# Performance work log

Measured on AMD Instinct MI355X. Metric: run time of the kernel, lower is better.

Reference implementation:

```python
import jax, jax.numpy as jnp
import numpy as np

LAMBDA = 25.0
MU = 25.0
NU = 1.0
ALPHA = 0.25
EPS = 1e-4
NUM_MATCHES = (20, 4)


def _cdist(x, y):
    # x: (B, L1, C), y: (B, L2, C) -> (B, L1, L2) euclidean distances
    x2 = jnp.sum(x * x, axis=-1)[..., :, None]
    y2 = jnp.sum(y * y, axis=-1)[..., None, :]
    d2 = x2 + y2 - 2.0 * jnp.einsum('blc,bmc->blm', x, y)
    return jnp.sqrt(jnp.maximum(d2, 0.0))


def _nearest_neighbors(input_maps, candidate_maps, distances, num_matches):
    # For each input location, its nearest candidate; then keep the
    # num_matches input locations with smallest NN distance, in original order.
    nn_dist = jnp.min(distances, axis=-1)    # (B, L1)
    nn_idx = jnp.argmin(distances, axis=-1)  # (B, L1)
    _, sel = jax.lax.top_k(-nn_dist, num_matches)  # (B, M) smallest distances
    sel = jnp.sort(sel, axis=1)  # restore original ordering of positions
    filtered_input = jnp.take_along_axis(input_maps, sel[..., None], axis=1)
    nn_sel = jnp.take_along_axis(nn_idx, sel, axis=1)
    filtered_candidate = jnp.take_along_axis(candidate_maps, nn_sel[..., None], axis=1)
    return filtered_input, filtered_candidate


def _mse(a, b):
    return jnp.mean((a - b) ** 2)


def _vicreg_loss(z_a, z_b):
    inv_loss = _mse(z_a, z_b)

    def var_loss(z):
        std = jnp.sqrt(jnp.var(z, axis=0, ddof=1) + EPS)
        return jnp.mean(jax.nn.relu(1.0 - std))

    def cov_loss(z):
        n, d = z.shape
        zc = z - jnp.mean(z, axis=0)
        cov = (zc.T @ zc) / (n - 1)
        off = cov - jnp.diag(jnp.diag(cov))
        return jnp.sum(off ** 2) / d

    v = 0.5 * (var_loss(z_a) + var_loss(z_b))
    c = cov_loss(z_a) + cov_loss(z_b)
    return LAMBDA * inv_loss + MU * v + NU * c


def _local_loss(z_global, z_local, grid_global, grid_local):
    B = z_global.shape[0]
    zg = z_global.reshape(B, -1, z_global.shape[-1])   # (B, Lg, C)
    zl = z_local.reshape(B, -1, z_local.shape[-1])     # (B, Ll, C)

    inv_loss = 0.0
    # feature-space NN
    gf, gn = _nearest_neighbors(zg, zl, _cdist(zg, zl), NUM_MATCHES[0])
    lf, ln = _nearest_neighbors(zl, zg, _cdist(zl, zg), NUM_MATCHES[1])
    inv_loss = inv_loss + (_mse(gf, gn) / 2 + _mse(lf, ln) / 2)

    # grid-space NN (distances from grids, gather from feature maps)
    gg = grid_global.reshape(B, -1, 2)
    gl = grid_local.reshape(B, -1, 2)
    gf, gn = _nearest_neighbors(zg, zl, _cdist(gg, gl), NUM_MATCHES[0])
    lf, ln = _nearest_neighbors(zl, zg, _cdist(gl, gg), NUM_MATCHES[1])
    inv_loss = inv_loss + (_mse(gf, gn) / 2 + _mse(lf, ln) / 2)

    return LAMBDA * inv_loss


def setup_inputs() -> dict:
    key = jax.random.key(0)
    ks = jax.random.split(key, 6)
    B, D, C = 32, 8192, 512
    return {
        'z_global': jax.random.normal(ks[0], (B, D), jnp.float32),
        'z_local': jax.random.normal(ks[1], (B, D), jnp.float32),
        'z_global_local_features': jax.random.normal(ks[2], (B, 24, 24, C), jnp.float32),
        'z_local_local_features': jax.random.normal(ks[3], (B, 16, 16, C), jnp.float32),
        'grid_global': jax.random.uniform(ks[4], (B, 24, 24, 2), jnp.float32),
        'grid_local': jax.random.uniform(ks[5], (B, 16, 16, 2), jnp.float32),
    }


def reference(z_global, z_local, z_global_local_features, z_local_local_features, grid_global, grid_local):
    global_loss = _vicreg_loss(z_global, z_local)
    local_loss = _local_loss(z_global_local_features, z_local_local_features, grid_global, grid_local)
    return ALPHA * global_loss + (1.0 - ALPHA) * local_loss
```

## Files before the change

### kernel.cpp

```cpp
#include <hip/hip_runtime.h>
#include <hip/hip_bf16.h>

#define BATCH 32
#define DZ    8192
#define LG    576
#define LL    256
#define CH    512

#define OFF_S      0
#define OFF_BSUM   8192
#define OFF_SELSUM 9472
#define OFF_NG     10496
#define OFF_NL     84224
#define OFF_ROWNN  116992
#define OFF_COLNN  264448
#define OFF_ABF    329984
#define OFF_BBF    19204352
#define WS_NEED    27592960

typedef __attribute__((ext_vector_type(8))) short bf16x8;
typedef __attribute__((ext_vector_type(4))) float f32x4;

__device__ __forceinline__ unsigned short f2bf(float x) {
  union { __hip_bfloat16 h; unsigned short u; } cv;
  cv.h = __float2bfloat16(x);
  return cv.u;
}

__global__ __launch_bounds__(256) void k_stats_gram(
    const float* __restrict__ za, const float* __restrict__ zb,
    double* __restrict__ bsum, float* __restrict__ S) {
  __shared__ float sred[4][5];
  int tid = threadIdx.x, lane = tid & 63, wv = tid >> 6;
  int blk = blockIdx.x;
  if (blk < 32) {
    int i = blk * 256 + tid;
    float sa = 0.f, qa = 0.f, sb = 0.f, qb = 0.f, si = 0.f;
    #pragma unroll 8
    for (int b = 0; b < BATCH; ++b) {
      float va = za[(size_t)b * DZ + i];
      float vb = zb[(size_t)b * DZ + i];
      sa += va; qa += va * va;
      sb += vb; qb += vb * vb;
      float d = va - vb; si += d * d;
    }
    float ssa = qa - sa * sa * (1.f / 32.f);
    float ssb = qb - sb * sb * (1.f / 32.f);
    float v0 = si;
    float v1 = fmaxf(0.f, 1.f - sqrtf(ssa * (1.f / 31.f) + 1e-4f));
    float v2 = fmaxf(0.f, 1.f - sqrtf(ssb * (1.f / 31.f) + 1e-4f));
    float v3 = ssa * ssa, v4 = ssb * ssb;
    for (int off = 32; off; off >>= 1) {
      v0 += __shfl_down(v0, off); v1 += __shfl_down(v1, off);
      v2 += __shfl_down(v2, off); v3 += __shfl_down(v3, off);
      v4 += __shfl_down(v4, off);
    }
    if (lane == 0) {
      sred[wv][0] = v0; sred[wv][1] = v1; sred[wv][2] = v2;
      sred[wv][3] = v3; sred[wv][4] = v4;
    }
    __syncthreads();
    if (tid < 5)
      bsum[blk * 5 + tid] =
          (double)(sred[0][tid] + sred[1][tid] + sred[2][tid] + sred[3][tid]);
  } else {
    int e = blk - 32;
    int zi = e >= 528; if (zi) e -= 528;
    const float* z = zi ? zb : za;
    float* Sz = S + zi * 1024;
    int p = 0, rem = e;
    while (rem >= 32 - p) { rem -= 32 - p; ++p; }
    int q = p + rem;
    const float4* zp = (const float4*)(z + (size_t)p * DZ);
    const float4* zq = (const float4*)(z + (size_t)q * DZ);
    float s = 0.f;
    #pragma unroll
    for (int ii = 0; ii < 8; ++ii) {
      int i = tid + ii * 256;
      float4 a = zp[i], b = zq[i];
      s += a.x * b.x + a.y * b.y + a.z * b.z + a.w * b.w;
    }
    for (int off = 32; off; off >>= 1) s += __shfl_down(s, off);
    if (lane == 0) sred[wv][0] = s;
    __syncthreads();
    if (tid == 0) {
      float r = sred[0][0] + sred[1][0] + sred[2][0] + sred[3][0];
      Sz[p * 32 + q] = r;
      if (p != q) Sz[q * 32 + p] = r;
    }
  }
}

__global__ __launch_bounds__(256) void k_prep(
    const float* __restrict__ zgf, const float* __restrict__ zlf,
    unsigned short* __restrict__ Abf, unsigned short* __restrict__ Bbf,
    float* __restrict__ ng, float* __restrict__ nl,
    unsigned long long* __restrict__ nnInit) {
  int row = blockIdx.x * 4 + (threadIdx.x >> 6);
  int lane = threadIdx.x & 63;
  if (lane == 0) nnInit[row] = ~0ull;
  const float* src; unsigned short* dst; float* nrm;
  if (row < BATCH * LG) {
    src = zgf + (size_t)row * CH; dst = Abf + (size_t)row * CH; nrm = ng + row;
  } else {
    int rr = row - BATCH * LG;
    src = zlf + (size_t)rr * CH; dst = Bbf + (size_t)rr * CH; nrm = nl + rr;
  }
  const float4* s4 = (const float4*)src;
  float4 v0 = s4[lane * 2], v1 = s4[lane * 2 + 1];
  float ss = v0.x * v0.x + v0.y * v0.y + v0.z * v0.z + v0.w * v0.w +
             v1.x * v1.x + v1.y * v1.y + v1.z * v1.z + v1.w * v1.w;
  union { unsigned short h[8]; uint4 u; } pk;
  pk.h[0] = f2bf(v0.x); pk.h[1] = f2bf(v0.y); pk.h[2] = f2bf(v0.z); pk.h[3] = f2bf(v0.w);
  pk.h[4] = f2bf(v1.x); pk.h[5] = f2bf(v1.y); pk.h[6] = f2bf(v1.z); pk.h[7] = f2bf(v1.w);
  *(uint4*)(dst + lane * 8) = pk.u;
  for (int off = 32; off; off >>= 1) ss += __shfl_down(ss, off);
  if (lane == 0) *nrm = ss;
}

__global__ __launch_bounds__(256) void k_feat_mfma(
    const unsigned short* __restrict__ Abf, const unsigned short* __restrict__ Bbf,
    const float* __restrict__ ng, const float* __restrict__ nl,
    unsigned long long* __restrict__ rowNN, unsigned long long* __restrict__ colNN) {
  const int b = blockIdx.z;
  const int row0 = blockIdx.x * 64;
  const int col0 = blockIdx.y * 64;
  const int tid = threadIdx.x;
  const int wave = tid >> 6, lane = tid & 63;
  const int m16 = lane & 15, quad = lane >> 4;
  const int wm = wave >> 1, wn = wave & 1;

  __shared__ unsigned short As[64][72];
  __shared__ unsigned short Bs[64][72];

  const unsigned short* Ag = Abf + ((size_t)(b * LG + row0)) * CH;
  const unsigned short* Bg = Bbf + ((size_t)(b * LL + col0)) * CH;

  const int sr = tid >> 2;
  const int sq = tid & 3;

  f32x4 acc[2][2] = {};

  for (int k0 = 0; k0 < CH; k0 += 64) {
    uint4 a0 = *(const uint4*)(Ag + (size_t)sr * CH + k0 + sq * 16);
    uint4 a1 = *(const uint4*)(Ag + (size_t)sr * CH + k0 + sq * 16 + 8);
    uint4 b0 = *(const uint4*)(Bg + (size_t)sr * CH + k0 + sq * 16);
    uint4 b1 = *(const uint4*)(Bg + (size_t)sr * CH + k0 + sq * 16 + 8);
    __syncthreads();
    *(uint4*)&As[sr][sq * 16] = a0; *(uint4*)&As[sr][sq * 16 + 8] = a1;
    *(uint4*)&Bs[sr][sq * 16] = b0; *(uint4*)&Bs[sr][sq * 16 + 8] = b1;
    __syncthreads();
    #pragma unroll
    for (int kk = 0; kk < 64; kk += 32) {
      bf16x8 af0 = *(const bf16x8*)&As[wm * 32 + m16][kk + quad * 8];
      bf16x8 af1 = *(const bf16x8*)&As[wm * 32 + 16 + m16][kk + quad * 8];
      bf16x8 bf0 = *(const bf16x8*)&Bs[wn * 32 + m16][kk + quad * 8];
      bf16x8 bf1 = *(const bf16x8*)&Bs[wn * 32 + 16 + m16][kk + quad * 8];
      acc[0][0] = __builtin_amdgcn_mfma_f32_16x16x32_bf16(af0, bf0, acc[0][0], 0, 0, 0);
      acc[0][1] = __builtin_amdgcn_mfma_f32_16x16x32_bf16(af0, bf1, acc[0][1], 0, 0, 0);
      acc[1][0] = __builtin_amdgcn_mfma_f32_16x16x32_bf16(af1, bf0, acc[1][0], 0, 0, 0);
      acc[1][1] = __builtin_amdgcn_mfma_f32_16x16x32_bf16(af1, bf1, acc[1][1], 0, 0, 0);
    }
  }

  float na[2][4], nb[2];
  #pragma unroll
  for (int i = 0; i < 2; ++i)
    #pragma unroll
    for (int r = 0; r < 4; ++r)
      na[i][r] = ng[b * LG + row0 + wm * 32 + i * 16 + quad * 4 + r];
  #pragma unroll
  for (int j = 0; j < 2; ++j)
    nb[j] = nl[b * LL + col0 + wn * 32 + j * 16 + m16];

  #pragma unroll
  for (int i = 0; i < 2; ++i) {
    #pragma unroll
    for (int r = 0; r < 4; ++r) {
      float d0 = fmaxf(na[i][r] + nb[0] - 2.f * acc[i][0][r], 0.f);
      float d1 = fmaxf(na[i][r] + nb[1] - 2.f * acc[i][1][r], 0.f);
      unsigned c0 = (unsigned)(col0 + wn * 32 + m16);
      unsigned long long p0 = (((unsigned long long)__float_as_uint(d0)) << 32) | c0;
      unsigned long long p1 = (((unsigned long long)__float_as_uint(d1)) << 32) | (c0 + 16);
      unsigned long long p = p0 < p1 ? p0 : p1;
      #pragma unroll
      for (int s = 1; s < 16; s <<= 1) {
        unsigned long long q = __shfl_xor(p, s);
        p = q < p ? q : p;
      }
      if (m16 == 0)
        atomicMin(&rowNN[(size_t)b * LG + row0 + wm * 32 + i * 16 + quad * 4 + r], p);
    }
  }
  #pragma unroll
  for (int j = 0; j < 2; ++j) {
    unsigned long long p = ~0ull;
    #pragma unroll
    for (int i = 0; i < 2; ++i) {
      #pragma unroll
      for (int r = 0; r < 4; ++r) {
        float d = fmaxf(na[i][r] + nb[j] - 2.f * acc[i][j][r], 0.f);
        unsigned rg = (unsigned)(row0 + wm * 32 + i * 16 + quad * 4 + r);
        unsigned long long pr = (((unsigned long long)__float_as_uint(d)) << 32) | rg;
        p = pr < p ? pr : p;
      }
    }
    unsigned long long q = __shfl_xor(p, 16); p = q < p ? q : p;
    q = __shfl_xor(p, 32); p = q < p ? q : p;
    if (quad == 0)
      atomicMin(&colNN[(size_t)b * LL + col0 + wn * 32 + j * 16 + m16], p);
  }
}

__global__ __launch_bounds__(64) void k_norms(
    const float* __restrict__ zgf, const float* __restrict__ zlf,
    float* __restrict__ ng, float* __restrict__ nl,
    unsigned long long* __restrict__ nnInit) {
  int r = blockIdx.x;
  if (threadIdx.x == 0) nnInit[r] = ~0ull;
  const float* src; float* dst;
  if (r < BATCH * LG) { src = zgf + (size_t)r * CH; dst = ng + r; }
  else { int rr = r - BATCH * LG; src = zlf + (size_t)rr * CH; dst = nl + rr; }
  float s = 0.f;
  for (int j = threadIdx.x; j < CH; j += 64) { float v = src[j]; s += v * v; }
  for (int off = 32; off > 0; off >>= 1) s += __shfl_down(s, off);
  if (threadIdx.x == 0) *dst = s;
}

__global__ __launch_bounds__(256) void k_feat_nn(
    const float* __restrict__ zgf, const float* __restrict__ zlf,
    const float* __restrict__ ng, const float* __restrict__ nl,
    unsigned long long* __restrict__ rowNN, unsigned long long* __restrict__ colNN) {
  const int b = blockIdx.z;
  const int row0 = blockIdx.x * 64;
  const int col0 = blockIdx.y * 128;
  const int tid = threadIdx.x;
  const int tx = tid & 15, ty = tid >> 4;
  __shared__ float As[64][20];
  __shared__ float Bs[128][20];
  __shared__ float Ds[64][130];
  const float* Ag = zgf + ((size_t)b * LG + row0) * CH;
  const float* Bg = zlf + ((size_t)b * LL + col0) * CH;
  float acc[4][8];
  #pragma unroll
  for (int i = 0; i < 4; ++i)
    #pragma unroll
    for (int j = 0; j < 8; ++j) acc[i][j] = 0.f;
  const int ar = tid >> 2;
  const int ak = (tid & 3) * 4;
  for (int k0 = 0; k0 < CH; k0 += 16) {
    float4 av  = *(const float4*)(Ag + (size_t)ar * CH + k0 + ak);
    float4 bv0 = *(const float4*)(Bg + (size_t)ar * CH + k0 + ak);
    float4 bv1 = *(const float4*)(Bg + (size_t)(ar + 64) * CH + k0 + ak);
    __syncthreads();
    *(float4*)&As[ar][ak] = av;
    *(float4*)&Bs[ar][ak] = bv0;
    *(float4*)&Bs[ar + 64][ak] = bv1;
    __syncthreads();
    #pragma unroll
    for (int k = 0; k < 16; ++k) {
      float a0 = As[ty][k], a1 = As[ty + 16][k], a2 = As[ty + 32][k], a3 = As[ty + 48][k];
      float bv[8];
      #pragma unroll
      for (int j = 0; j < 8; ++j) bv[j] = Bs[tx + 16 * j][k];
      #pragma unroll
      for (int j = 0; j < 8; ++j) {
        acc[0][j] += a0 * bv[j]; acc[1][j] += a1 * bv[j];
        acc[2][j] += a2 * bv[j]; acc[3][j] += a3 * bv[j];
      }
    }
  }
  float ngr[4], nlc[8];
  #pragma unroll
  for (int i = 0; i < 4; ++i) ngr[i] = ng[b * LG + row0 + ty + 16 * i];
  #pragma unroll
  for (int j = 0; j < 8; ++j) nlc[j] = nl[b * LL + col0 + tx + 16 * j];
  #pragma unroll
  for (int i = 0; i < 4; ++i)
    #pragma unroll
    for (int j = 0; j < 8; ++j)
      Ds[ty + 16 * i][tx + 16 * j] = fmaxf(ngr[i] + nlc[j] - 2.f * acc[i][j], 0.f);
  __syncthreads();
  if (tid < 64) {
    unsigned long long best = ~0ull;
    for (int c = 0; c < 128; ++c) {
      unsigned long long p =
          ((unsigned long long)__float_as_uint(Ds[tid][c]) << 32) | (unsigned)(col0 + c);
      best = p < best ? p : best;
    }
    atomicMin(&rowNN[(size_t)b * LG + row0 + tid], best);
  } else if (tid < 192) {
    int c = tid - 64;
    unsigned long long best = ~0ull;
    for (int r = 0; r < 64; ++r) {
      unsigned long long p =
          ((unsigned long long)__float_as_uint(Ds[r][c]) << 32) | (unsigned)(row0 + r);
      best = p < best ? p : best;
    }
    atomicMin(&colNN[(size_t)b * LL + col0 + c], best);
  }
}

struct SelSmem {
  unsigned long long keys[LG];
  unsigned int nnm[LG];
  float cxy[2 * LG];
  unsigned int plist[40];
  unsigned int cnt;
  float fred[4];
};

template <int V>
__device__ __forceinline__ void sel_case(
    SelSmem& sm, int b,
    const float* __restrict__ zgf, const float* __restrict__ zlf,
    const float* __restrict__ gg, const float* __restrict__ gl,
    const unsigned long long* __restrict__ rowNN,
    const unsigned long long* __restrict__ colNN,
    double* __restrict__ selsum) {
  constexpr bool GDIR = (V == 0 || V == 2);
  constexpr int L1 = GDIR ? LG : LL;
  constexpr int L2 = GDIR ? LL : LG;
  constexpr int M  = GDIR ? 20 : 4;
  constexpr int NR = (L1 + 255) / 256;
  const float* fin  = GDIR ? zgf + (size_t)b * LG * CH : zlf + (size_t)b * LL * CH;
  const float* fcan = GDIR ? zlf + (size_t)b * LL * CH : zgf + (size_t)b * LG * CH;
  int tid = threadIdx.x, lane = tid & 63, wv = tid >> 6;
  if (tid == 0) sm.cnt = 0;

  if constexpr (V < 2) {
    const unsigned long long* src =
        (V == 0) ? rowNN + (size_t)b * LG : colNN + (size_t)b * LL;
    #pragma unroll
    for (int s = 0; s < NR; ++s) {
      int l = tid + s * 256;
      if (l < L1) {
        unsigned long long p = src[l];
        sm.keys[l] = (p & 0xFFFFFFFF00000000ull) | (unsigned)l;
        sm.nnm[l] = (unsigned)(p & 0xFFFFFFFFu);
      }
    }
  } else {
    const float* gin  = (V == 2) ? gg + (size_t)b * LG * 2 : gl + (size_t)b * LL * 2;
    const float* gcan = (V == 2) ? gl + (size_t)b * LL * 2 : gg + (size_t)b * LG * 2;
    #pragma unroll
    for (int s = 0; s < (2 * L2 + 255) / 256; ++s) {
      int i = tid + s * 256;
      if (i < 2 * L2) sm.cxy[i] = gcan[i];
    }
    __syncthreads();
    float x[NR], y[NR], bd[NR];
    unsigned bi[NR];
    #pragma unroll
    for (int s = 0; s < NR; ++s) {
      int l = tid + s * 256;
      x[s] = (l < L1) ? gin[2 * l] : 0.f;
      y[s] = (l < L1) ? gin[2 * l + 1] : 0.f;
      bd[s] = 3.4e38f; bi[s] = 0;
    }
    const float2* c2 = (const float2*)sm.cxy;
    for (int m2 = 0; m2 < L2; m2 += 8) {
      float2 cc[8];
      #pragma unroll
      for (int u = 0; u < 8; ++u) cc[u] = c2[m2 + u];
      #pragma unroll
      for (int u = 0; u < 8; ++u)
        #pragma unroll
        for (int s = 0; s < NR; ++s) {
          float dx = x[s] - cc[u].x, dy = y[s] - cc[u].y;
          float d2 = dx * dx + dy * dy;
          if (d2 < bd[s]) { bd[s] = d2; bi[s] = (unsigned)(m2 + u); }
        }
    }
    #pragma unroll
    for (int s = 0; s < NR; ++s) {
      int l = tid + s * 256;
      if (l < L1) {
        sm.keys[l] = ((unsigned long long)__float_as_uint(bd[s]) << 32) | (unsigned)l;
        sm.nnm[l] = bi[s];
      }
    }
  }
  __syncthreads();

  unsigned long long myk[NR];
  int rk[NR];
  #pragma unroll
  for (int s = 0; s < NR; ++s) {
    int l = tid + s * 256;
    myk[s] = (l < L1) ? sm.keys[l] : ~0ull;
    rk[s] = 0;
  }
  for (int j = 0; j < L1; j += 8) {
    unsigned long long kk[8];
    #pragma unroll
    for (int u = 0; u < 8; ++u) kk[u] = sm.keys[j + u];
    #pragma unroll
    for (int u = 0; u < 8; ++u)
      #pragma unroll
      for (int s = 0; s < NR; ++s) rk[s] += (kk[u] < myk[s]) ? 1 : 0;
  }
  #pragma unroll
  for (int s = 0; s < NR; ++s) {
    int l = tid + s * 256;
    if (l < L1 && rk[s] < M) {
      unsigned slot = atomicAdd(&sm.cnt, 1u);
      sm.plist[2 * slot] = (unsigned)l;
      sm.plist[2 * slot + 1] = sm.nnm[l];
    }
  }
  __syncthreads();

  float part = 0.f;
  #pragma unroll
  for (int rr = 0; rr < M / 4; ++rr) {
    int r = wv + rr * 4;
    const float4* a4 = (const float4*)(fin + (size_t)sm.plist[2 * r] * CH);
    const float4* c4 = (const float4*)(fcan + (size_t)sm.plist[2 * r + 1] * CH);
    float4 xa = a4[lane * 2], xb = a4[lane * 2 + 1];
    float4 ya = c4[lane * 2], yb = c4[lane * 2 + 1];
    float d0 = xa.x - ya.x, d1 = xa.y - ya.y, d2 = xa.z - ya.z, d3 = xa.w - ya.w;
    float d4 = xb.x - yb.x, d5 = xb.y - yb.y, d6 = xb.z - yb.z, d7 = xb.w - yb.w;
    part += d0 * d0 + d1 * d1 + d2 * d2 + d3 * d3 +
            d4 * d4 + d5 * d5 + d6 * d6 + d7 * d7;
  }
  for (int s = 32; s; s >>= 1) part += __shfl_down(part, s);
  if (lane == 0) sm.fred[wv] = part;
  __syncthreads();
  if (tid == 0)
    selsum[V * 32 + b] = (double)(sm.fred[0] + sm.fred[1] + sm.fred[2] + sm.fred[3]);
}

__global__ __launch_bounds__(256) void k_sel(
    const float* __restrict__ zgf, const float* __restrict__ zlf,
    const float* __restrict__ gg, const float* __restrict__ gl,
    const unsigned long long* __restrict__ rowNN,
    const unsigned long long* __restrict__ colNN,
    double* __restrict__ selsum) {
  __shared__ SelSmem sm;
  int b = blockIdx.x;
  switch (blockIdx.y) {
    case 0: sel_case<0>(sm, b, zgf, zlf, gg, gl, rowNN, colNN, selsum); break;
    case 1: sel_case<1>(sm, b, zgf, zlf, gg, gl, rowNN, colNN, selsum); break;
    case 2: sel_case<2>(sm, b, zgf, zlf, gg, gl, rowNN, colNN, selsum); break;
    default: sel_case<3>(sm, b, zgf, zlf, gg, gl, rowNN, colNN, selsum); break;
  }
}

__global__ __launch_bounds__(64) void k_final(
    const double* __restrict__ bsum, const double* __restrict__ selsum,
    const float* __restrict__ S, float* __restrict__ out) {
  __shared__ float t[2][32];
  __shared__ double sacc[5];
  __shared__ double smf[4];
  int lane = threadIdx.x;
  #pragma unroll
  for (int zi = 0; zi < 2; ++zi) {
    if (lane < 32) {
      float tp = 0.f;
      for (int bb = 0; bb < 32; ++bb) tp += S[zi * 1024 + lane * 32 + bb];
      t[zi][lane] = tp * (1.f / 32.f);
    }
  }
  if (lane < 5) {
    double s = 0.0;
    for (int blk = 0; blk < 32; ++blk) s += bsum[blk * 5 + lane];
    sacc[lane] = s;
  }
  if (lane >= 8 && lane < 12) {
    int v = lane - 8;
    double s = 0.0;
    for (int bb = 0; bb < 32; ++bb) s += selsum[v * 32 + bb];
    smf[v] = s;
  }
  __syncthreads();
  double total[2];
  #pragma unroll
  for (int zi = 0; zi < 2; ++zi) {
    float u = 0.f;
    for (int bb = 0; bb < 32; ++bb) u += t[zi][bb];
    u *= (1.f / 32.f);
    double s = 0.0;
    for (int e = lane; e < 1024; e += 64) {
      int p = e >> 5, q = e & 31;
      float G = S[zi * 1024 + e] - t[zi][p] - t[zi][q] + u;
      s += (double)G * (double)G;
    }
    for (int off = 32; off; off >>= 1) s += __shfl_down(s, off);
    total[zi] = s;
  }
  if (lane == 0) {
    double inv_g = sacc[0] / (32.0 * 8192.0);
    double v = 0.5 * (sacc[1] + sacc[2]) / 8192.0;
    double c = (total[0] - sacc[3] + total[1] - sacc[4]) / (961.0 * 8192.0);
    double gloss = 25.0 * inv_g + 25.0 * v + c;
    double mfg = smf[0] / (32.0 * 20.0 * 512.0);
    double mfl = smf[1] / (32.0 * 4.0 * 512.0);
    double mgg = smf[2] / (32.0 * 20.0 * 512.0);
    double mgl = smf[3] / (32.0 * 4.0 * 512.0);
    double lloss = 25.0 * (0.5 * (mfg + mfl) + 0.5 * (mgg + mgl));
    out[0] = (float)(0.25 * gloss + 0.75 * lloss);
  }
}

extern "C" void kernel_launch(void* const* d_in, const int* in_sizes, int n_in,
                              void* d_out, int out_size, void* d_ws, size_t ws_size,
                              hipStream_t stream) {
  const float* zg  = (const float*)d_in[0];
  const float* zl  = (const float*)d_in[1];
  const float* zgf = (const float*)d_in[2];
  const float* zlf = (const float*)d_in[3];
  const float* gg  = (const float*)d_in[4];
  const float* glo = (const float*)d_in[5];

  char* ws = (char*)d_ws;
  float* S       = (float*)(ws + OFF_S);
  double* bsum   = (double*)(ws + OFF_BSUM);
  double* selsum = (double*)(ws + OFF_SELSUM);
  float* ng = (float*)(ws + OFF_NG);
  float* nl = (float*)(ws + OFF_NL);
  unsigned long long* rowNN = (unsigned long long*)(ws + OFF_ROWNN);
  unsigned long long* colNN = (unsigned long long*)(ws + OFF_COLNN);
  unsigned short* Abf = (unsigned short*)(ws + OFF_ABF);
  unsigned short* Bbf = (unsigned short*)(ws + OFF_BBF);

  k_stats_gram<<<32 + 1056, 256, 0, stream>>>(zg, zl, bsum, S);

  if (ws_size >= WS_NEED) {
    k_prep<<<(BATCH * (LG + LL)) / 4, 256, 0, stream>>>(zgf, zlf, Abf, Bbf, ng, nl, rowNN);
    k_feat_mfma<<<dim3(LG / 64, LL / 64, BATCH), 256, 0, stream>>>(Abf, Bbf, ng, nl, rowNN, colNN);
  } else {
    k_norms<<<BATCH * (LG + LL), 64, 0, stream>>>(zgf, zlf, ng, nl, rowNN);
    k_feat_nn<<<dim3(LG / 64, LL / 128, BATCH), 256, 0, stream>>>(zgf, zlf, ng, nl, rowNN, colNN);
  }
  k_sel<<<dim3(BATCH, 4), 256, 0, stream>>>(zgf, zlf, gg, glo, rowNN, colNN, selsum);
  k_final<<<1, 64, 0, stream>>>(bsum, selsum, S, (float*)d_out);
}
```

Before: 169.4 us.

## Fuse front-end kernels, run grid-space selection early, finalize in last sel block

Merges the global stats/gram, bf16 prep/norms and the grid-space NN selection cases into one large front kernel. The grid-space selection does not depend on the feature GEMM, so it now runs alongside independent work. The final reduction moves into the selection kernel, where the last block to finish (tracked by an atomic counter) computes the output. This removes two launches and shortens the dependency chain, at the cost of a heavier heterogeneous kernel and atomic/fence ordering logic. The grid-space cases appear to pass nnInit as rowNN/colNN, which the same kernel is also initializing, so that path needs checking.

Result: slower. 183.6 us (+8.4%).

```diff
diff --git a/kernel.cpp b/kernel.cpp
--- a/kernel.cpp
+++ b/kernel.cpp
@@ -10,13 +10,14 @@
 #define OFF_S      0
 #define OFF_BSUM   8192
 #define OFF_SELSUM 9472
-#define OFF_NG     10496
-#define OFF_NL     84224
-#define OFF_ROWNN  116992
-#define OFF_COLNN  264448
-#define OFF_ABF    329984
-#define OFF_BBF    19204352
-#define WS_NEED    27592960
+#define OFF_DONE   10496
+#define OFF_NG     10560
+#define OFF_NL     84288
+#define OFF_ROWNN  117056
+#define OFF_COLNN  264512
+#define OFF_ABF    330048
+#define OFF_BBF    19204416
+#define WS_NEED    27593024
 
 typedef __attribute__((ext_vector_type(8))) short bf16x8;
 typedef __attribute__((ext_vector_type(4))) float f32x4;
@@ -25,280 +26,6 @@
   union { __hip_bfloat16 h; unsigned short u; } cv;
   cv.h = __float2bfloat16(x);
   return cv.u;
-}
-
-__global__ __launch_bounds__(256) void k_stats_gram(
-    const float* __restrict__ za, const float* __restrict__ zb,
-    double* __restrict__ bsum, float* __restrict__ S) {
-  __shared__ float sred[4][5];
-  int tid = threadIdx.x, lane = tid & 63, wv = tid >> 6;
-  int blk = blockIdx.x;
-  if (blk < 32) {
-    int i = blk * 256 + tid;
-    float sa = 0.f, qa = 0.f, sb = 0.f, qb = 0.f, si = 0.f;
-    #pragma unroll 8
-    for (int b = 0; b < BATCH; ++b) {
-      float va = za[(size_t)b * DZ + i];
-      float vb = zb[(size_t)b * DZ + i];
-      sa += va; qa += va * va;
-      sb += vb; qb += vb * vb;
-      float d = va - vb; si += d * d;
-    }
-    float ssa = qa - sa * sa * (1.f / 32.f);
-    float ssb = qb - sb * sb * (1.f / 32.f);
-    float v0 = si;
-    float v1 = fmaxf(0.f, 1.f - sqrtf(ssa * (1.f / 31.f) + 1e-4f));
-    float v2 = fmaxf(0.f, 1.f - sqrtf(ssb * (1.f / 31.f) + 1e-4f));
-    float v3 = ssa * ssa, v4 = ssb * ssb;
-    for (int off = 32; off; off >>= 1) {
-      v0 += __shfl_down(v0, off); v1 += __shfl_down(v1, off);
-      v2 += __shfl_down(v2, off); v3 += __shfl_down(v3, off);
-      v4 += __shfl_down(v4, off);
-    }
-    if (lane == 0) {
-      sred[wv][0] = v0; sred[wv][1] = v1; sred[wv][2] = v2;
-      sred[wv][3] = v3; sred[wv][4] = v4;
-    }
-    __syncthreads();
-    if (tid < 5)
-      bsum[blk * 5 + tid] =
-          (double)(sred[0][tid] + sred[1][tid] + sred[2][tid] + sred[3][tid]);
-  } else {
-    int e = blk - 32;
-    int zi = e >= 528; if (zi) e -= 528;
-    const float* z = zi ? zb : za;
-    float* Sz = S + zi * 1024;
-    int p = 0, rem = e;
-    while (rem >= 32 - p) { rem -= 32 - p; ++p; }
-    int q = p + rem;
-    const float4* zp = (const float4*)(z + (size_t)p * DZ);
-    const float4* zq = (const float4*)(z + (size_t)q * DZ);
-    float s = 0.f;
-    #pragma unroll
-    for (int ii = 0; ii < 8; ++ii) {
-      int i = tid + ii * 256;
-      float4 a = zp[i], b = zq[i];
-      s += a.x * b.x + a.y * b.y + a.z * b.z + a.w * b.w;
-    }
-    for (int off = 32; off; off >>= 1) s += __shfl_down(s, off);
-    if (lane == 0) sred[wv][0] = s;
-    __syncthreads();
-    if (tid == 0) {
-      float r = sred[0][0] + sred[1][0] + sred[2][0] + sred[3][0];
-      Sz[p * 32 + q] = r;
-      if (p != q) Sz[q * 32 + p] = r;
-    }
-  }
-}
-
-__global__ __launch_bounds__(256) void k_prep(
-    const float* __restrict__ zgf, const float* __restrict__ zlf,
-    unsigned short* __restrict__ Abf, unsigned short* __restrict__ Bbf,
-    float* __restrict__ ng, float* __restrict__ nl,
-    unsigned long long* __restrict__ nnInit) {
-  int row = blockIdx.x * 4 + (threadIdx.x >> 6);
-  int lane = threadIdx.x & 63;
-  if (lane == 0) nnInit[row] = ~0ull;
-  const float* src; unsigned short* dst; float* nrm;
-  if (row < BATCH * LG) {
-    src = zgf + (size_t)row * CH; dst = Abf + (size_t)row * CH; nrm = ng + row;
-  } else {
-    int rr = row - BATCH * LG;
-    src = zlf + (size_t)rr * CH; dst = Bbf + (size_t)rr * CH; nrm = nl + rr;
-  }
-  const float4* s4 = (const float4*)src;
-  float4 v0 = s4[lane * 2], v1 = s4[lane * 2 + 1];
-  float ss = v0.x * v0.x + v0.y * v0.y + v0.z * v0.z + v0.w * v0.w +
-             v1.x * v1.x + v1.y * v1.y + v1.z * v1.z + v1.w * v1.w;
-  union { unsigned short h[8]; uint4 u; } pk;
-  pk.h[0] = f2bf(v0.x); pk.h[1] = f2bf(v0.y); pk.h[2] = f2bf(v0.z); pk.h[3] = f2bf(v0.w);
-  pk.h[4] = f2bf(v1.x); pk.h[5] = f2bf(v1.y); pk.h[6] = f2bf(v1.z); pk.h[7] = f2bf(v1.w);
-  *(uint4*)(dst + lane * 8) = pk.u;
-  for (int off = 32; off; off >>= 1) ss += __shfl_down(ss, off);
-  if (lane == 0) *nrm = ss;
-}
-
-__global__ __launch_bounds__(256) void k_feat_mfma(
-    const unsigned short* __restrict__ Abf, const unsigned short* __restrict__ Bbf,
-    const float* __restrict__ ng, const float* __restrict__ nl,
-    unsigned long long* __restrict__ rowNN, unsigned long long* __restrict__ colNN) {
-  const int b = blockIdx.z;
-  const int row0 = blockIdx.x * 64;
-  const int col0 = blockIdx.y * 64;
-  const int tid = threadIdx.x;
-  const int wave = tid >> 6, lane = tid & 63;
-  const int m16 = lane & 15, quad = lane >> 4;
-  const int wm = wave >> 1, wn = wave & 1;
-
-  __shared__ unsigned short As[64][72];
-  __shared__ unsigned short Bs[64][72];
-
-  const unsigned short* Ag = Abf + ((size_t)(b * LG + row0)) * CH;
-  const unsigned short* Bg = Bbf + ((size_t)(b * LL + col0)) * CH;
-
-  const int sr = tid >> 2;
-  const int sq = tid & 3;
-
-  f32x4 acc[2][2] = {};
-
-  for (int k0 = 0; k0 < CH; k0 += 64) {
-    uint4 a0 = *(const uint4*)(Ag + (size_t)sr * CH + k0 + sq * 16);
-    uint4 a1 = *(const uint4*)(Ag + (size_t)sr * CH + k0 + sq * 16 + 8);
-    uint4 b0 = *(const uint4*)(Bg + (size_t)sr * CH + k0 + sq * 16);
-    uint4 b1 = *(const uint4*)(Bg + (size_t)sr * CH + k0 + sq * 16 + 8);
-    __syncthreads();
-    *(uint4*)&As[sr][sq * 16] = a0; *(uint4*)&As[sr][sq * 16 + 8] = a1;
-    *(uint4*)&Bs[sr][sq * 16] = b0; *(uint4*)&Bs[sr][sq * 16 + 8] = b1;
-    __syncthreads();
-    #pragma unroll
-    for (int kk = 0; kk < 64; kk += 32) {
-      bf16x8 af0 = *(const bf16x8*)&As[wm * 32 + m16][kk + quad * 8];
-      bf16x8 af1 = *(const bf16x8*)&As[wm * 32 + 16 + m16][kk + quad * 8];
-      bf16x8 bf0 = *(const bf16x8*)&Bs[wn * 32 + m16][kk + quad * 8];
-      bf16x8 bf1 = *(const bf16x8*)&Bs[wn * 32 + 16 + m16][kk + quad * 8];
-      acc[0][0] = __builtin_amdgcn_mfma_f32_16x16x32_bf16(af0, bf0, acc[0][0], 0, 0, 0);
-      acc[0][1] = __builtin_amdgcn_mfma_f32_16x16x32_bf16(af0, bf1, acc[0][1], 0, 0, 0);
-      acc[1][0] = __builtin_amdgcn_mfma_f32_16x16x32_bf16(af1, bf0, acc[1][0], 0, 0, 0);
-      acc[1][1] = __builtin_amdgcn_mfma_f32_16x16x32_bf16(af1, bf1, acc[1][1], 0, 0, 0);
-    }
-  }
-
-  float na[2][4], nb[2];
-  #pragma unroll
-  for (int i = 0; i < 2; ++i)
-    #pragma unroll
-    for (int r = 0; r < 4; ++r)
-      na[i][r] = ng[b * LG + row0 + wm * 32 + i * 16 + quad * 4 + r];
-  #pragma unroll
-  for (int j = 0; j < 2; ++j)
-    nb[j] = nl[b * LL + col0 + wn * 32 + j * 16 + m16];
-
-  #pragma unroll
-  for (int i = 0; i < 2; ++i) {
-    #pragma unroll
-    for (int r = 0; r < 4; ++r) {
-      float d0 = fmaxf(na[i][r] + nb[0] - 2.f * acc[i][0][r], 0.f);
-      float d1 = fmaxf(na[i][r] + nb[1] - 2.f * acc[i][1][r], 0.f);
-      unsigned c0 = (unsigned)(col0 + wn * 32 + m16);
-      unsigned long long p0 = (((unsigned long long)__float_as_uint(d0)) << 32) | c0;
-      unsigned long long p1 = (((unsigned long long)__float_as_uint(d1)) << 32) | (c0 + 16);
-      unsigned long long p = p0 < p1 ? p0 : p1;
-      #pragma unroll
-      for (int s = 1; s < 16; s <<= 1) {
-        unsigned long long q = __shfl_xor(p, s);
-        p = q < p ? q : p;
-      }
-      if (m16 == 0)
-        atomicMin(&rowNN[(size_t)b * LG + row0 + wm * 32 + i * 16 + quad * 4 + r], p);
-    }
-  }
-  #pragma unroll
-  for (int j = 0; j < 2; ++j) {
-    unsigned long long p = ~0ull;
-    #pragma unroll
-    for (int i = 0; i < 2; ++i) {
-      #pragma unroll
-      for (int r = 0; r < 4; ++r) {
-        float d = fmaxf(na[i][r] + nb[j] - 2.f * acc[i][j][r], 0.f);
-        unsigned rg = (unsigned)(row0 + wm * 32 + i * 16 + quad * 4 + r);
-        unsigned long long pr = (((unsigned long long)__float_as_uint(d)) << 32) | rg;
-        p = pr < p ? pr : p;
-      }
-    }
-    unsigned long long q = __shfl_xor(p, 16); p = q < p ? q : p;
-    q = __shfl_xor(p, 32); p = q < p ? q : p;
-    if (quad == 0)
-      atomicMin(&colNN[(size_t)b * LL + col0 + wn * 32 + j * 16 + m16], p);
-  }
-}
-
-__global__ __launch_bounds__(64) void k_norms(
-    const float* __restrict__ zgf, const float* __restrict__ zlf,
-    float* __restrict__ ng, float* __restrict__ nl,
-    unsigned long long* __restrict__ nnInit) {
-  int r = blockIdx.x;
-  if (threadIdx.x == 0) nnInit[r] = ~0ull;
-  const float* src; float* dst;
-  if (r < BATCH * LG) { src = zgf + (size_t)r * CH; dst = ng + r; }
-  else { int rr = r - BATCH * LG; src = zlf + (size_t)rr * CH; dst = nl + rr; }
-  float s = 0.f;
-  for (int j = threadIdx.x; j < CH; j += 64) { float v = src[j]; s += v * v; }
-  for (int off = 32; off > 0; off >>= 1) s += __shfl_down(s, off);
-  if (threadIdx.x == 0) *dst = s;
-}
-
-__global__ __launch_bounds__(256) void k_feat_nn(
-    const float* __restrict__ zgf, const float* __restrict__ zlf,
-    const float* __restrict__ ng, const float* __restrict__ nl,
-    unsigned long long* __restrict__ rowNN, unsigned long long* __restrict__ colNN) {
-  const int b = blockIdx.z;
-  const int row0 = blockIdx.x * 64;
-  const int col0 = blockIdx.y * 128;
-  const int tid = threadIdx.x;
-  const int tx = tid & 15, ty = tid >> 4;
-  __shared__ float As[64][20];
-  __shared__ float Bs[128][20];
-  __shared__ float Ds[64][130];
-  const float* Ag = zgf + ((size_t)b * LG + row0) * CH;
-  const float* Bg = zlf + ((size_t)b * LL + col0) * CH;
-  float acc[4][8];
-  #pragma unroll
-  for (int i = 0; i < 4; ++i)
-    #pragma unroll
-    for (int j = 0; j < 8; ++j) acc[i][j] = 0.f;
-  const int ar = tid >> 2;
-  const int ak = (tid & 3) * 4;
-  for (int k0 = 0; k0 < CH; k0 += 16) {
-    float4 av  = *(const float4*)(Ag + (size_t)ar * CH + k0 + ak);
-    float4 bv0 = *(const float4*)(Bg + (size_t)ar * CH + k0 + ak);
-    float4 bv1 = *(const float4*)(Bg + (size_t)(ar + 64) * CH + k0 + ak);
-    __syncthreads();
-    *(float4*)&As[ar][ak] = av;
-    *(float4*)&Bs[ar][ak] = bv0;
-    *(float4*)&Bs[ar + 64][ak] = bv1;
-    __syncthreads();
-    #pragma unroll
-    for (int k = 0; k < 16; ++k) {
-      float a0 = As[ty][k], a1 = As[ty + 16][k], a2 = As[ty + 32][k], a3 = As[ty + 48][k];
-      float bv[8];
-      #pragma unroll
-      for (int j = 0; j < 8; ++j) bv[j] = Bs[tx + 16 * j][k];
-      #pragma unroll
-      for (int j = 0; j < 8; ++j) {
-        acc[0][j] += a0 * bv[j]; acc[1][j] += a1 * bv[j];
-        acc[2][j] += a2 * bv[j]; acc[3][j] += a3 * bv[j];
-      }
-    }
-  }
-  float ngr[4], nlc[8];
-  #pragma unroll
-  for (int i = 0; i < 4; ++i) ngr[i] = ng[b * LG + row0 + ty + 16 * i];
-  #pragma unroll
-  for (int j = 0; j < 8; ++j) nlc[j] = nl[b * LL + col0 + tx + 16 * j];
-  #pragma unroll
-  for (int i = 0; i < 4; ++i)
-    #pragma unroll
-    for (int j = 0; j < 8; ++j)
-      Ds[ty + 16 * i][tx + 16 * j] = fmaxf(ngr[i] + nlc[j] - 2.f * acc[i][j], 0.f);
-  __syncthreads();
-  if (tid < 64) {
-    unsigned long long best = ~0ull;
-    for (int c = 0; c < 128; ++c) {
-      unsigned long long p =
-          ((unsigned long long)__float_as_uint(Ds[tid][c]) << 32) | (unsigned)(col0 + c);
-      best = p < best ? p : best;
-    }
-    atomicMin(&rowNN[(size_t)b * LG + row0 + tid], best);
-  } else if (tid < 192) {
-    int c = tid - 64;
-    unsigned long long best = ~0ull;
-    for (int r = 0; r < 64; ++r) {
-      unsigned long long p =
-          ((unsigned long long)__float_as_uint(Ds[r][c]) << 32) | (unsigned)(row0 + r);
-      best = p < best ? p : best;
-    }
-    atomicMin(&colNN[(size_t)b * LL + col0 + c], best);
-  }
 }
 
 struct SelSmem {
@@ -431,75 +158,350 @@
     selsum[V * 32 + b] = (double)(sm.fred[0] + sm.fred[1] + sm.fred[2] + sm.fred[3]);
 }
 
+__global__ __launch_bounds__(256) void k_front(
+    const float* __restrict__ za, const float* __restrict__ zb,
+    const float* __restrict__ zgf, const float* __restrict__ zlf,
+    const float* __restrict__ gg, const float* __restrict__ gl,
+    double* __restrict__ bsum, float* __restrict__ S,
+    unsigned short* __restrict__ Abf, unsigned short* __restrict__ Bbf,
+    float* __restrict__ ng, float* __restrict__ nl,
+    unsigned long long* __restrict__ nnInit,
+    double* __restrict__ selsum, unsigned* __restrict__ done, int do_bf16) {
+  __shared__ float sred[4][8];
+  __shared__ SelSmem sm;
+  int tid = threadIdx.x, lane = tid & 63, wv = tid >> 6;
+  int blk = blockIdx.x;
+
+  if (blk < 32) {
+    if (blk == 0 && tid == 0) *done = 0u;
+    int i = blk * 256 + tid;
+    float sa = 0.f, qa = 0.f, sb = 0.f, qb = 0.f, si = 0.f;
+    #pragma unroll 8
+    for (int b = 0; b < BATCH; ++b) {
+      float va = za[(size_t)b * DZ + i];
+      float vb = zb[(size_t)b * DZ + i];
+      sa += va; qa += va * va;
+      sb += vb; qb += vb * vb;
+      float d = va - vb; si += d * d;
+    }
+    float ssa = qa - sa * sa * (1.f / 32.f);
+    float ssb = qb - sb * sb * (1.f / 32.f);
+    float v0 = si;
+    float v1 = fmaxf(0.f, 1.f - sqrtf(ssa * (1.f / 31.f) + 1e-4f));
+    float v2 = fmaxf(0.f, 1.f - sqrtf(ssb * (1.f / 31.f) + 1e-4f));
+    float v3 = ssa * ssa, v4 = ssb * ssb;
+    for (int off = 32; off; off >>= 1) {
+      v0 += __shfl_down(v0, off); v1 += __shfl_down(v1, off);
+      v2 += __shfl_down(v2, off); v3 += __shfl_down(v3, off);
+      v4 += __shfl_down(v4, off);
+    }
+    if (lane == 0) {
+      sred[wv][0] = v0; sred[wv][1] = v1; sred[wv][2] = v2;
+      sred[wv][3] = v3; sred[wv][4] = v4;
+    }
+    __syncthreads();
+    if (tid < 5)
+      bsum[blk * 5 + tid] =
+          (double)(sred[0][tid] + sred[1][tid] + sred[2][tid] + sred[3][tid]);
+  } else if (blk < 1088) {
+    int e = blk - 32;
+    int zi = e >= 528; if (zi) e -= 528;
+    const float* z = zi ? zb : za;
+    float* Sz = S + zi * 1024;
+    int p = 0, rem = e;
+    while (rem >= 32 - p) { rem -= 32 - p; ++p; }
+    int q = p + rem;
+    const float4* zp = (const float4*)(z + (size_t)p * DZ);
+    const float4* zq = (const float4*)(z + (size_t)q * DZ);
+    float s = 0.f;
+    #pragma unroll
+    for (int ii = 0; ii < 8; ++ii) {
+      int i = tid + ii * 256;
+      float4 a = zp[i], b = zq[i];
+      s += a.x * b.x + a.y * b.y + a.z * b.z + a.w * b.w;
+    }
+    for (int off = 32; off; off >>= 1) s += __shfl_down(s, off);
+    if (lane == 0) sred[wv][0] = s;
+    __syncthreads();
+    if (tid == 0) {
+      float r = sred[0][0] + sred[1][0] + sred[2][0] + sred[3][0];
+      Sz[p * 32 + q] = r;
+      if (p != q) Sz[q * 32 + p] = r;
+    }
+  } else if (blk < 7744) {
+    int row = (blk - 1088) * 4 + wv;
+    if (lane == 0) nnInit[row] = ~0ull;
+    const float* src; unsigned short* dst; float* nrm;
+    if (row < BATCH * LG) {
+      src = zgf + (size_t)row * CH; dst = Abf + (size_t)row * CH; nrm = ng + row;
+    } else {
+      int rr = row - BATCH * LG;
+      src = zlf + (size_t)rr * CH; dst = Bbf + (size_t)rr * CH; nrm = nl + rr;
+    }
+    const float4* s4 = (const float4*)src;
+    float4 v0 = s4[lane * 2], v1 = s4[lane * 2 + 1];
+    float ss = v0.x * v0.x + v0.y * v0.y + v0.z * v0.z + v0.w * v0.w +
+               v1.x * v1.x + v1.y * v1.y + v1.z * v1.z + v1.w * v1.w;
+    if (do_bf16) {
+      union { unsigned short h[8]; uint4 u; } pk;
+      pk.h[0] = f2bf(v0.x); pk.h[1] = f2bf(v0.y); pk.h[2] = f2bf(v0.z); pk.h[3] = f2bf(v0.w);
+      pk.h[4] = f2bf(v1.x); pk.h[5] = f2bf(v1.y); pk.h[6] = f2bf(v1.z); pk.h[7] = f2bf(v1.w);
+      *(uint4*)(dst + lane * 8) = pk.u;
+    }
+    for (int off = 32; off; off >>= 1) ss += __shfl_down(ss, off);
+    if (lane == 0) *nrm = ss;
+  } else {
+    int e = blk - 7744;
+    int b = e & 31;
+    if (e >> 5)
+      sel_case<3>(sm, b, zgf, zlf, gg, gl, nnInit, nnInit, selsum);
+    else
+      sel_case<2>(sm, b, zgf, zlf, gg, gl, nnInit, nnInit, selsum);
+  }
+}
+
+__global__ __launch_bounds__(256) void k_feat_mfma(
+    const unsigned short* __restrict__ Abf, const unsigned short* __restrict__ Bbf,
+    const float* __restrict__ ng, const float* __restrict__ nl,
+    unsigned long long* __restrict__ rowNN, unsigned long long* __restrict__ colNN) {
+  const int b = blockIdx.z;
+  const int row0 = blockIdx.x * 64;
+  const int col0 = blockIdx.y * 64;
+  const int tid = threadIdx.x;
+  const int wave = tid >> 6, lane = tid & 63;
+  const int m16 = lane & 15, quad = lane >> 4;
+  const int wm = wave >> 1, wn = wave & 1;
+
+  __shared__ unsigned short As[64][72];
+  __shared__ unsigned short Bs[64][72];
+
+  const unsigned short* Ag = Abf + ((size_t)(b * LG + row0)) * CH;
+  const unsigned short* Bg = Bbf + ((size_t)(b * LL + col0)) * CH;
+
+  const int sr = tid >> 2;
+  const int sq = tid & 3;
+
+  f32x4 acc[2][2] = {};
+
+  for (int k0 = 0; k0 < CH; k0 += 64) {
+    uint4 a0 = *(const uint4*)(Ag + (size_t)sr * CH + k0 + sq * 16);
+    uint4 a1 = *(const uint4*)(Ag + (size_t)sr * CH + k0 + sq * 16 + 8);
+    uint4 b0 = *(const uint4*)(Bg + (size_t)sr * CH + k0 + sq * 16);
+    uint4 b1 = *(const uint4*)(Bg + (size_t)sr * CH + k0 + sq * 16 + 8);
+    __syncthreads();
+    *(uint4*)&As[sr][sq * 16] = a0; *(uint4*)&As[sr][sq * 16 + 8] = a1;
+    *(uint4*)&Bs[sr][sq * 16] = b0; *(uint4*)&Bs[sr][sq * 16 + 8] = b1;
+    __syncthreads();
+    #pragma unroll
+    for (int kk = 0; kk < 64; kk += 32) {
+      bf16x8 af0 = *(const bf16x8*)&As[wm * 32 + m16][kk + quad * 8];
+      bf16x8 af1 = *(const bf16x8*)&As[wm * 32 + 16 + m16][kk + quad * 8];
+      bf16x8 bf0 = *(const bf16x8*)&Bs[wn * 32 + m16][kk + quad * 8];
+      bf16x8 bf1 = *(const bf16x8*)&Bs[wn * 32 + 16 + m16][kk + quad * 8];
+      acc[0][0] = __builtin_amdgcn_mfma_f32_16x16x32_bf16(af0, bf0, acc[0][0], 0, 0, 0);
+      acc[0][1] = __builtin_amdgcn_mfma_f32_16x16x32_bf16(af0, bf1, acc[0][1], 0, 0, 0);
+      acc[1][0] = __builtin_amdgcn_mfma_f32_16x16x32_bf16(af1, bf0, acc[1][0], 0, 0, 0);
+      acc[1][1] = __builtin_amdgcn_mfma_f32_16x16x32_bf16(af1, bf1, acc[1][1], 0, 0, 0);
+    }
+  }
+
+  float na[2][4], nb[2];
+  #pragma unroll
+  for (int i = 0; i < 2; ++i)
+    #pragma unroll
+    for (int r = 0; r < 4; ++r)
+      na[i][r] = ng[b * LG + row0 + wm * 32 + i * 16 + quad * 4 + r];
+  #pragma unroll
+  for (int j = 0; j < 2; ++j)
+    nb[j] = nl[b * LL + col0 + wn * 32 + j * 16 + m16];
+
+  #pragma unroll
+  for (int i = 0; i < 2; ++i) {
+    #pragma unroll
+    for (int r = 0; r < 4; ++r) {
+      float d0 = fmaxf(na[i][r] + nb[0] - 2.f * acc[i][0][r], 0.f);
+      float d1 = fmaxf(na[i][r] + nb[1] - 2.f * acc[i][1][r], 0.f);
+      unsigned c0 = (unsigned)(col0 + wn * 32 + m16);
+      unsigned long long p0 = (((unsigned long long)__float_as_uint(d0)) << 32) | c0;
+      unsigned long long p1 = (((unsigned long long)__float_as_uint(d1)) << 32) | (c0 + 16);
+      unsigned long long p = p0 < p1 ? p0 : p1;
+      #pragma unroll
+      for (int s = 1; s < 16; s <<= 1) {
+        unsigned long long q = __shfl_xor(p, s);
+        p = q < p ? q : p;
+      }
+      if (m16 == 0)
+        atomicMin(&rowNN[(size_t)b * LG + row0 + wm * 32 + i * 16 + quad * 4 + r], p);
+    }
+  }
+  #pragma unroll
+  for (int j = 0; j < 2; ++j) {
+    unsigned long long p = ~0ull;
+    #pragma unroll
+    for (int i = 0; i < 2; ++i) {
+      #pragma unroll
+      for (int r = 0; r < 4; ++r) {
+        float d = fmaxf(na[i][r] + nb[j] - 2.f * acc[i][j][r], 0.f);
+        unsigned rg = (unsigned)(row0 + wm * 32 + i * 16 + quad * 4 + r);
+        unsigned long long pr = (((unsigned long long)__float_as_uint(d)) << 32) | rg;
+        p = pr < p ? pr : p;
+      }
+    }
+    unsigned long long q = __shfl_xor(p, 16); p = q < p ? q : p;
+    q = __shfl_xor(p, 32); p = q < p ? q : p;
+    if (quad == 0)
+      atomicMin(&colNN[(size_t)b * LL + col0 + wn * 32 + j * 16 + m16], p);
+  }
+}
+
+__global__ __launch_bounds__(256) void k_feat_nn(
+    const float* __restrict__ zgf, const float* __restrict__ zlf,
+    const float* __restrict__ ng, const float* __restrict__ nl,
+    unsigned long long* __restrict__ rowNN, unsigned long long* __restrict__ colNN) {
+  const int b = blockIdx.z;
+  const int row0 = blockIdx.x * 64;
+  const int col0 = blockIdx.y * 128;
+  const int tid = threadIdx.x;
+  const int tx = tid & 15, ty = tid >> 4;
+  __shared__ float As[64][20];
+  __shared__ float Bs[128][20];
+  __shared__ float Ds[64][130];
+  const float* Ag = zgf + ((size_t)b * LG + row0) * CH;
+  const float* Bg = zlf + ((size_t)b * LL + col0) * CH;
+  float acc[4][8];
+  #pragma unroll
+  for (int i = 0; i < 4; ++i)
+    #pragma unroll
+    for (int j = 0; j < 8; ++j) acc[i][j] = 0.f;
+  const int ar = tid >> 2;
+  const int ak = (tid & 3) * 4;
+  for (int k0 = 0; k0 < CH; k0 += 16) {
+    float4 av  = *(const float4*)(Ag + (size_t)ar * CH + k0 + ak);
+    float4 bv0 = *(const float4*)(Bg + (size_t)ar * CH + k0 + ak);
+    float4 bv1 = *(const float4*)(Bg + (size_t)(ar + 64) * CH + k0 + ak);
+    __syncthreads();
+    *(float4*)&As[ar][ak] = av;
+    *(float4*)&Bs[ar][ak] = bv0;
+    *(float4*)&Bs[ar + 64][ak] = bv1;
+    __syncthreads();
+    #pragma unroll
+    for (int k = 0; k < 16; ++k) {
+      float a0 = As[ty][k], a1 = As[ty + 16][k], a2 = As[ty + 32][k], a3 = As[ty + 48][k];
+      float bv[8];
+      #pragma unroll
+      for (int j = 0; j < 8; ++j) bv[j] = Bs[tx + 16 * j][k];
+      #pragma unroll
+      for (int j = 0; j < 8; ++j) {
+        acc[0][j] += a0 * bv[j]; acc[1][j] += a1 * bv[j];
+        acc[2][j] += a2 * bv[j]; acc[3][j] += a3 * bv[j];
+      }
+    }
+  }
+  float ngr[4], nlc[8];
+  #pragma unroll
+  for (int i = 0; i < 4; ++i) ngr[i] = ng[b * LG + row0 + ty + 16 * i];
+  #pragma unroll
+  for (int j = 0; j < 8; ++j) nlc[j] = nl[b * LL + col0 + tx + 16 * j];
+  #pragma unroll
+  for (int i = 0; i < 4; ++i)
+    #pragma unroll
+    for (int j = 0; j < 8; ++j)
+      Ds[ty + 16 * i][tx + 16 * j] = fmaxf(ngr[i] + nlc[j] - 2.f * acc[i][j], 0.f);
+  __syncthreads();
+  if (tid < 64) {
+    unsigned long long best = ~0ull;
+    for (int c = 0; c < 128; ++c) {
+      unsigned long long p =
+          ((unsigned long long)__float_as_uint(Ds[tid][c]) << 32) | (unsigned)(col0 + c);
+      best = p < best ? p : best;
+    }
+    atomicMin(&rowNN[(size_t)b * LG + row0 + tid], best);
+  } else if (tid < 192) {
+    int c = tid - 64;
+    unsigned long long best = ~0ull;
+    for (int r = 0; r < 64; ++r) {
+      unsigned long long p =
+          ((unsigned long long)__float_as_uint(Ds[r][c]) << 32) | (unsigned)(row0 + r);
+      best = p < best ? p : best;
+    }
+    atomicMin(&colNN[(size_t)b * LL + col0 + c], best);
+  }
+}
+
 __global__ __launch_bounds__(256) void k_sel(
     const float* __restrict__ zgf, const float* __restrict__ zlf,
     const float* __restrict__ gg, const float* __restrict__ gl,
     const unsigned long long* __restrict__ rowNN,
     const unsigned long long* __restrict__ colNN,
-    double* __restrict__ selsum) {
+    double* __restrict__ selsum, const double* __restrict__ bsum,
+    const float* __restrict__ S, unsigned* __restrict__ done,
+    float* __restrict__ out) {
   __shared__ SelSmem sm;
   int b = blockIdx.x;
-  switch (blockIdx.y) {
-    case 0: sel_case<0>(sm, b, zgf, zlf, gg, gl, rowNN, colNN, selsum); break;
-    case 1: sel_case<1>(sm, b, zgf, zlf, gg, gl, rowNN, colNN, selsum); break;
-    case 2: sel_case<2>(sm, b, zgf, zlf, gg, gl, rowNN, colNN, selsum); break;
-    default: sel_case<3>(sm, b, zgf, zlf, gg, gl, rowNN, colNN, selsum); break;
-  }
-}
-
-__global__ __launch_bounds__(64) void k_final(
-    const double* __restrict__ bsum, const double* __restrict__ selsum,
-    const float* __restrict__ S, float* __restrict__ out) {
+  if (blockIdx.y == 0)
+    sel_case<0>(sm, b, zgf, zlf, gg, gl, rowNN, colNN, selsum);
+  else
+    sel_case<1>(sm, b, zgf, zlf, gg, gl, rowNN, colNN, selsum);
+
+  __shared__ unsigned isLast;
   __shared__ float t[2][32];
   __shared__ double sacc[5];
   __shared__ double smf[4];
-  int lane = threadIdx.x;
-  #pragma unroll
-  for (int zi = 0; zi < 2; ++zi) {
-    if (lane < 32) {
+  __shared__ double totred[2];
+  int tid = threadIdx.x, lane = tid & 63, wv = tid >> 6;
+  if (tid == 0) {
+    __threadfence();
+    unsigned old = __hip_atomic_fetch_add(done, 1u, __ATOMIC_ACQ_REL,
+                                          __HIP_MEMORY_SCOPE_AGENT);
+    isLast = (old == 63u) ? 1u : 0u;
+  }
+  __syncthreads();
+  if (isLast) {
+    __threadfence();
+    if (tid < 64) {
+      int zi = tid >> 5, p = tid & 31;
       float tp = 0.f;
-      for (int bb = 0; bb < 32; ++bb) tp += S[zi * 1024 + lane * 32 + bb];
-      t[zi][lane] = tp * (1.f / 32.f);
-    }
-  }
-  if (lane < 5) {
-    double s = 0.0;
-    for (int blk = 0; blk < 32; ++blk) s += bsum[blk * 5 + lane];
-    sacc[lane] = s;
-  }
-  if (lane >= 8 && lane < 12) {
-    int v = lane - 8;
-    double s = 0.0;
-    for (int bb = 0; bb < 32; ++bb) s += selsum[v * 32 + bb];
-    smf[v] = s;
-  }
-  __syncthreads();
-  double total[2];
-  #pragma unroll
-  for (int zi = 0; zi < 2; ++zi) {
-    float u = 0.f;
-    for (int bb = 0; bb < 32; ++bb) u += t[zi][bb];
-    u *= (1.f / 32.f);
-    double s = 0.0;
-    for (int e = lane; e < 1024; e += 64) {
-      int p = e >> 5, q = e & 31;
-      float G = S[zi * 1024 + e] - t[zi][p] - t[zi][q] + u;
-      s += (double)G * (double)G;
-    }
-    for (int off = 32; off; off >>= 1) s += __shfl_down(s, off);
-    total[zi] = s;
-  }
-  if (lane == 0) {
-    double inv_g = sacc[0] / (32.0 * 8192.0);
-    double v = 0.5 * (sacc[1] + sacc[2]) / 8192.0;
-    double c = (total[0] - sacc[3] + total[1] - sacc[4]) / (961.0 * 8192.0);
-    double gloss = 25.0 * inv_g + 25.0 * v + c;
-    double mfg = smf[0] / (32.0 * 20.0 * 512.0);
-    double mfl = smf[1] / (32.0 * 4.0 * 512.0);
-    double mgg = smf[2] / (32.0 * 20.0 * 512.0);
-    double mgl = smf[3] / (32.0 * 4.0 * 512.0);
-    double lloss = 25.0 * (0.5 * (mfg + mfl) + 0.5 * (mgg + mgl));
-    out[0] = (float)(0.25 * gloss + 0.75 * lloss);
+      for (int bb = 0; bb < 32; ++bb) tp += S[zi * 1024 + p * 32 + bb];
+      t[zi][p] = tp * (1.f / 32.f);
+    } else if (tid < 69) {
+      int k = tid - 64;
+      double s = 0.0;
+      for (int blk = 0; blk < 32; ++blk) s += bsum[blk * 5 + k];
+      sacc[k] = s;
+    } else if (tid >= 72 && tid < 76) {
+      int v = tid - 72;
+      double s = 0.0;
+      for (int bb = 0; bb < 32; ++bb) s += selsum[v * 32 + bb];
+      smf[v] = s;
+    }
+    __syncthreads();
+    if (wv < 2) {
+      int zi = wv;
+      float u = 0.f;
+      for (int bb = 0; bb < 32; ++bb) u += t[zi][bb];
+      u *= (1.f / 32.f);
+      double s = 0.0;
+      for (int e = lane; e < 1024; e += 64) {
+        int p = e >> 5, q = e & 31;
+        float G = S[zi * 1024 + e] - t[zi][p] - t[zi][q] + u;
+        s += (double)G * (double)G;
+      }
+      for (int off = 32; off; off >>= 1) s += __shfl_down(s, off);
+      if (lane == 0) totred[zi] = s;
+    }
+    __syncthreads();
+    if (tid == 0) {
+      double inv_g = sacc[0] / (32.0 * 8192.0);
+      double v = 0.5 * (sacc[1] + sacc[2]) / 8192.0;
+      double c = (totred[0] - sacc[3] + totred[1] - sacc[4]) / (961.0 * 8192.0);
+      double gloss = 25.0 * inv_g + 25.0 * v + c;
+      double mfg = smf[0] / (32.0 * 20.0 * 512.0);
+      double mfl = smf[1] / (32.0 * 4.0 * 512.0);
+      double mgg = smf[2] / (32.0 * 20.0 * 512.0);
+      double mgl = smf[3] / (32.0 * 4.0 * 512.0);
+      double lloss = 25.0 * (0.5 * (mfg + mfl) + 0.5 * (mgg + mgl));
+      out[0] = (float)(0.25 * gloss + 0.75 * lloss);
+    }
   }
 }
 
@@ -517,6 +519,7 @@
   float* S       = (float*)(ws + OFF_S);
   double* bsum   = (double*)(ws + OFF_BSUM);
   double* selsum = (double*)(ws + OFF_SELSUM);
+  unsigned* done = (unsigned*)(ws + OFF_DONE);
   float* ng = (float*)(ws + OFF_NG);
   float* nl = (float*)(ws + OFF_NL);
   unsigned long long* rowNN = (unsigned long long*)(ws + OFF_ROWNN);
@@ -524,15 +527,17 @@
   unsigned short* Abf = (unsigned short*)(ws + OFF_ABF);
   unsigned short* Bbf = (unsigned short*)(ws + OFF_BBF);
 
-  k_stats_gram<<<32 + 1056, 256, 0, stream>>>(zg, zl, bsum, S);
-
-  if (ws_size >= WS_NEED) {
-    k_prep<<<(BATCH * (LG + LL)) / 4, 256, 0, stream>>>(zgf, zlf, Abf, Bbf, ng, nl, rowNN);
-    k_feat_mfma<<<dim3(LG / 64, LL / 64, BATCH), 256, 0, stream>>>(Abf, Bbf, ng, nl, rowNN, colNN);
+  int do_bf16 = (ws_size >= WS_NEED) ? 1 : 0;
+
+  k_front<<<7808, 256, 0, stream>>>(zg, zl, zgf, zlf, gg, glo, bsum, S,
+                                    Abf, Bbf, ng, nl, rowNN, selsum, done, do_bf16);
+  if (do_bf16) {
+    k_feat_mfma<<<dim3(LG / 64, LL / 64, BATCH), 256, 0, stream>>>(
+        Abf, Bbf, ng, nl, rowNN, colNN);
   } else {
-    k_norms<<<BATCH * (LG + LL), 64, 0, stream>>>(zgf, zlf, ng, nl, rowNN);
-    k_feat_nn<<<dim3(LG / 64, LL / 128, BATCH), 256, 0, stream>>>(zgf, zlf, ng, nl, rowNN, colNN);
-  }
-  k_sel<<<dim3(BATCH, 4), 256, 0, stream>>>(zgf, zlf, gg, glo, rowNN, colNN, selsum);
-  k_final<<<1, 64, 0, stream>>>(bsum, selsum, S, (float*)d_out);
-}
+    k_feat_nn<<<dim3(LG / 64, LL / 128, BATCH), 256, 0, stream>>>(
+        zgf, zlf, ng, nl, rowNN, colNN);
+  }
+  k_sel<<<dim3(BATCH, 2), 256, 0, stream>>>(zgf, zlf, gg, glo, rowNN, colNN,
+                                            selsum, bsum, S, done, (float*)d_out);
+}
```
